# Performance work log

Hardware: AMD Instinct MI355X
Metric: run time of the kernel (lower is better)

The kernel has to match this reference:

```python
import jax, jax.numpy as jnp
import numpy as np

N = 50000      # nodes
E = 800000     # edges (avg degree 16)
G = 1024       # graphs in batch
C = 128        # hidden / interaction channels
FIN = 16       # num_node_features
FE = 3         # num_edge_features
L = 3          # num_interactions
CUTOFF = 10.0
LOG2 = float(np.log(2.0))
BN_EPS = 1e-5

def ssp(v):
    # ShiftedSoftplus: softplus(x) - log(2)
    return jax.nn.softplus(v) - LOG2

def setup_inputs() -> dict:
    key = jax.random.key(0)
    ks = jax.random.split(key, 24)
    s = 0.05
    inp = {}
    inp["x"] = jax.random.normal(ks[0], (N, FIN), jnp.float32)
    inp["edge_index"] = jax.random.randint(ks[1], (2, E), 0, N, dtype=jnp.int32)
    inp["edge_weight"] = jax.random.uniform(ks[2], (E,), jnp.float32) * CUTOFF
    inp["edge_attr"] = jax.random.normal(ks[3], (E, FE), jnp.float32)
    inp["batch"] = jnp.sort(jax.random.randint(ks[4], (N,), 0, G, dtype=jnp.int32))
    # node embedding (node_data='x'): Linear(FIN,C) -> Linear(C,C)
    inp["W_l1"] = jax.random.normal(ks[5], (FIN, C), jnp.float32) * s
    inp["b_l1"] = jnp.zeros((C,), jnp.float32)
    inp["W_l2"] = jax.random.normal(ks[6], (C, C), jnp.float32) * s
    inp["b_l2"] = jnp.zeros((C,), jnp.float32)
    # BatchNorm1d affine params
    inp["bn_g"] = jnp.ones((C,), jnp.float32)
    inp["bn_b"] = jnp.zeros((C,), jnp.float32)
    # L stacked interaction layers (SchNet-style CFConv)
    inp["Wi_in"] = jax.random.normal(ks[7], (L, C, C), jnp.float32) * s
    inp["bi_in"] = jnp.zeros((L, C), jnp.float32)
    inp["We1"] = jax.random.normal(ks[8], (L, FE, C), jnp.float32) * s
    inp["be1"] = jnp.zeros((L, C), jnp.float32)
    inp["We2"] = jax.random.normal(ks[9], (L, C, C), jnp.float32) * s
    inp["be2"] = jnp.zeros((L, C), jnp.float32)
    inp["Wi_out"] = jax.random.normal(ks[10], (L, C, C), jnp.float32) * s
    inp["bi_out"] = jnp.zeros((L, C), jnp.float32)
    # GeneralReadOutLayer (128,'sum',32,1): pool -> Linear(128,32)+SSP -> Linear(32,1)+SSP
    inp["W_r1"] = jax.random.normal(ks[11], (C, 32), jnp.float32) * s
    inp["b_r1"] = jnp.zeros((32,), jnp.float32)
    inp["W_r2"] = jax.random.normal(ks[12], (32, 1), jnp.float32) * s
    inp["b_r2"] = jnp.zeros((1,), jnp.float32)
    return inp

def _forward(x, edge_weight, edge_attr,
             W_l1, b_l1, W_l2, b_l2, bn_g, bn_b,
             Wi_in, bi_in, We1, be1, We2, be2, Wi_out, bi_out,
             W_r1, b_r1, W_r2, b_r2, edge_index, batch):
    src, dst = edge_index[0], edge_index[1]
    # node embedding: Linear -> Linear
    h = (x @ W_l1 + b_l1) @ W_l2 + b_l2                   # [N, C]
    # BatchNorm1d (training-mode batch stats over nodes)
    mu = jnp.mean(h, axis=0)
    var = jnp.var(h, axis=0)
    h = (h - mu) * jax.lax.rsqrt(var + BN_EPS) * bn_g + bn_b
    # cosine cutoff envelope on edge distances
    env = 0.5 * (jnp.cos(edge_weight * (jnp.pi / CUTOFF)) + 1.0)  # [E]
    # GeoResNet: residual stack of interactions
    for i in range(L):
        filt = ssp(edge_attr @ We1[i] + be1[i]) @ We2[i] + be2[i]   # [E, C]
        hin = h @ Wi_in[i] + bi_in[i]                               # [N, C]
        msg = hin[src] * filt * env[:, None]                        # [E, C] gather
        agg = jax.ops.segment_sum(msg, dst, num_segments=N)         # [N, C] scatter
        h = h + ssp(agg @ Wi_out[i] + bi_out[i])
    # GeneralReadOutLayer: segment 'sum' pool then MLP with SSP
    hg = jax.ops.segment_sum(h, batch, num_segments=G)              # [G, C]
    out = ssp(hg @ W_r1 + b_r1)
    out = ssp(out @ W_r2 + b_r2)                                    # [G, 1]
    return out.reshape(-1)                                          # [G]

def reference(x, edge_index, edge_weight, edge_attr, batch,
              W_l1, b_l1, W_l2, b_l2, bn_g, bn_b,
              Wi_in, bi_in, We1, be1, We2, be2, Wi_out, bi_out,
              W_r1, b_r1, W_r2, b_r2):
    return _forward(x, edge_weight, edge_attr,
                    W_l1, b_l1, W_l2, b_l2, bn_g, bn_b,
                    Wi_in, bi_in, We1, be1, We2, be2, Wi_out, bi_out,
                    W_r1, b_r1, W_r2, b_r2, edge_index, batch)
```

## Files before the change

### kernel.cpp

```cpp
#include <hip/hip_runtime.h>
#include <math.h>

#define N_NODES 50000
#define N_EDGES 800000
#define N_GRAPH 1024
#define CDIM 128
#define FINDIM 16
#define NL 3
#define WTP 132

using short8  = __attribute__((ext_vector_type(8))) short;
using floatx4 = __attribute__((ext_vector_type(4))) float;

__device__ __forceinline__ float sspf(float x) {
    return fmaxf(x, 0.0f) + __logf(1.0f + __expf(-fabsf(x))) - 0.6931471805599453f;
}

__device__ __forceinline__ unsigned short f2bf(float f) {
    unsigned int u = __float_as_uint(f);
    u = u + 0x7FFFu + ((u >> 16) & 1u);
    return (unsigned short)(u >> 16);
}

__device__ __forceinline__ float bf2f(unsigned short h) {
    return __uint_as_float((unsigned int)h << 16);
}

__device__ __forceinline__ short8 ldfrag(const unsigned short* WT, int c, int k0) {
    const uint2* p = (const uint2*)(WT + c * WTP + k0);
    short8 r;
    *(uint2*)&r       = p[0];
    *((uint2*)&r + 1) = p[1];
    return r;
}

__global__ void k_fuse(const float* __restrict__ Wl1, const float* __restrict__ bl1,
                       const float* __restrict__ Wl2, const float* __restrict__ bl2,
                       float* __restrict__ Wf, float* __restrict__ bfv) {
    for (int o = threadIdx.x; o < FINDIM * CDIM + CDIM; o += 256) {
        if (o < FINDIM * CDIM) {
            int f = o >> 7, c = o & 127;
            float s = 0.f;
            for (int k = 0; k < CDIM; ++k) s += Wl1[f * CDIM + k] * Wl2[k * CDIM + c];
            Wf[o] = s;
        } else {
            int c = o - FINDIM * CDIM;
            float s = bl2[c];
            for (int k = 0; k < CDIM; ++k) s += bl1[k] * Wl2[k * CDIM + c];
            bfv[c] = s;
        }
    }
}

__global__ void k_embed_bn(const float* __restrict__ x, const float* __restrict__ Wf,
                           const float* __restrict__ bfv, float* __restrict__ h,
                           float* __restrict__ bnsum) {
    __shared__ float wfs[FINDIM * CDIM];
    __shared__ float bfs[CDIM];
    __shared__ float sd[512];
    for (int o = threadIdx.x; o < FINDIM * CDIM; o += 256) wfs[o] = Wf[o];
    if (threadIdx.x < CDIM) bfs[threadIdx.x] = bfv[threadIdx.x];
    __syncthreads();
    int c = threadIdx.x & 127;
    int half = threadIdx.x >> 7;
    float s1 = 0.f, s2 = 0.f;
    for (int base = blockIdx.x * 2; base < N_NODES; base += gridDim.x * 2) {
        int n = base + half;
        if (n < N_NODES) {
            float s = bfs[c];
            const float* xp = x + (size_t)n * FINDIM;
#pragma unroll
            for (int f = 0; f < FINDIM; ++f) s += xp[f] * wfs[f * CDIM + c];
            h[(size_t)n * CDIM + c] = s;
            s1 += s; s2 += s * s;
        }
    }
    sd[threadIdx.x] = s1; sd[256 + threadIdx.x] = s2;
    __syncthreads();
    if (threadIdx.x < 128) {
        atomicAdd(&bnsum[threadIdx.x], sd[threadIdx.x] + sd[threadIdx.x + 128]);
        atomicAdd(&bnsum[128 + threadIdx.x], sd[256 + threadIdx.x] + sd[256 + threadIdx.x + 128]);
    }
}

__global__ void k_bnapply(float* __restrict__ h, unsigned short* __restrict__ hb,
                          const float* __restrict__ bnsum,
                          const float* __restrict__ g, const float* __restrict__ b) {
    const float invN = 1.0f / (float)N_NODES;
    for (size_t i = (size_t)blockIdx.x * 256 + threadIdx.x; i < (size_t)N_NODES * CDIM;
         i += (size_t)gridDim.x * 256) {
        int c = (int)(i & 127);
        float mu  = bnsum[c] * invN;
        float var = bnsum[128 + c] * invN - mu * mu;
        float sc  = g[c] * rsqrtf(var + 1e-5f);
        float v = (h[i] - mu) * sc + b[c];
        h[i] = v;
        hb[i] = f2bf(v);
    }
}

__global__ void k_hist(const int* __restrict__ edst, int* __restrict__ deg) {
    int e = blockIdx.x * 256 + threadIdx.x;
    if (e < N_EDGES) atomicAdd(&deg[edst[e]], 1);
}

#define SCAN_T 1024
#define CHUNK 49
__global__ void k_scan(const int* __restrict__ deg, int* __restrict__ row_ptr) {
    __shared__ int part[SCAN_T];
    int t = threadIdx.x;
    int begin = t * CHUNK;
    int end   = begin + CHUNK; if (end > N_NODES) end = N_NODES;
    int s = 0;
    for (int i = begin; i < end && i < N_NODES; ++i) s += deg[i];
    part[t] = s;
    __syncthreads();
    for (int off = 1; off < SCAN_T; off <<= 1) {
        int v = (t >= off) ? part[t - off] : 0;
        __syncthreads();
        part[t] += v;
        __syncthreads();
    }
    int run = (t == 0) ? 0 : part[t - 1];
    for (int i = begin; i < end && i < N_NODES; ++i) { row_ptr[i] = run; run += deg[i]; }
    if (t == SCAN_T - 1) row_ptr[N_NODES] = run;
}

__global__ void k_scatter(const int* __restrict__ edst, const int* __restrict__ row_ptr,
                          int* __restrict__ cnt, int* __restrict__ perm) {
    int e = blockIdx.x * 256 + threadIdx.x;
    if (e < N_EDGES) {
        int d = edst[e];
        int pos = row_ptr[d] + atomicAdd(&cnt[d], 1);
        perm[pos] = e;
    }
}

__global__ void k_pack(const int* __restrict__ perm, const int* __restrict__ esrc,
                       const int* __restrict__ edst, const float* __restrict__ ew,
                       const float* __restrict__ ea,
                       int2* __restrict__ rmeta, float4* __restrict__ rea) {
    int i = blockIdx.x * 256 + threadIdx.x;
    if (i < N_EDGES) {
        int e = perm[i];
        float w = ew[e];
        float env = 0.5f * (__cosf(w * 0.31415926535897932f) + 1.0f);
        rmeta[i] = make_int2(esrc[e], edst[e]);
        rea[i] = make_float4(ea[(size_t)e * 3], ea[(size_t)e * 3 + 1], ea[(size_t)e * 3 + 2], env);
    }
}

__global__ __launch_bounds__(256, 2) void k_ngemm_in(const unsigned short* __restrict__ hb,
                                                     const float* __restrict__ B,
                                                     const float* __restrict__ bias,
                                                     unsigned short* __restrict__ hinb) {
    __shared__ unsigned short WT[128 * WTP];
    __shared__ float bs[CDIM];
    for (int o = threadIdx.x; o < CDIM * CDIM; o += 256) {
        int k = o >> 7, c = o & 127;
        WT[c * WTP + k] = f2bf(B[o]);
    }
    if (threadIdx.x < CDIM) bs[threadIdx.x] = bias[threadIdx.x];
    __syncthreads();

    int lane = threadIdx.x & 63, wave = threadIdx.x >> 6;
    int m = lane & 15, q = lane >> 4;
    int rb = blockIdx.x * 64 + wave * 16;
    int row = rb + m;
    if (row > N_NODES - 1) row = N_NODES - 1;

    floatx4 acc[8];
#pragma unroll
    for (int nt = 0; nt < 8; ++nt) acc[nt] = (floatx4){0.f, 0.f, 0.f, 0.f};

#pragma unroll
    for (int kb = 0; kb < 4; ++kb) {
        int k0 = kb * 32 + q * 8;
        short8 af = *(const short8*)(hb + (size_t)row * CDIM + k0);
#pragma unroll
        for (int nt = 0; nt < 8; ++nt) {
            short8 bf = ldfrag(WT, nt * 16 + m, k0);
            acc[nt] = __builtin_amdgcn_mfma_f32_16x16x32_bf16(af, bf, acc[nt], 0, 0, 0);
        }
    }
#pragma unroll
    for (int nt = 0; nt < 8; ++nt) {
        int c = nt * 16 + m;
#pragma unroll
        for (int r = 0; r < 4; ++r) {
            int orow = rb + q * 4 + r;
            if (orow < N_NODES)
                hinb[(size_t)orow * CDIM + c] = f2bf(acc[nt][r] + bs[c]);
        }
    }
}

template <int ZERO, int POOL>
__global__ __launch_bounds__(256, 2) void k_ngemm_out(float* __restrict__ agg,
                                                      const float* __restrict__ B,
                                                      const float* __restrict__ bias,
                                                      float* __restrict__ h,
                                                      unsigned short* __restrict__ hb,
                                                      const int* __restrict__ batch,
                                                      float* __restrict__ hg) {
    __shared__ unsigned short WT[128 * WTP];
    __shared__ float bs[CDIM];
    for (int o = threadIdx.x; o < CDIM * CDIM; o += 256) {
        int k = o >> 7, c = o & 127;
        WT[c * WTP + k] = f2bf(B[o]);
    }
    if (threadIdx.x < CDIM) bs[threadIdx.x] = bias[threadIdx.x];
    __syncthreads();

    int lane = threadIdx.x & 63, wave = threadIdx.x >> 6;
    int m = lane & 15, q = lane >> 4;
    int rb = blockIdx.x * 64 + wave * 16;
    int row = rb + m;
    if (row > N_NODES - 1) row = N_NODES - 1;

    floatx4 acc[8];
#pragma unroll
    for (int nt = 0; nt < 8; ++nt) acc[nt] = (floatx4){0.f, 0.f, 0.f, 0.f};

#pragma unroll
    for (int kb = 0; kb < 4; ++kb) {
        int k0 = kb * 32 + q * 8;
        const float* ap = agg + (size_t)row * CDIM + k0;
        float4 lo = *(const float4*)ap;
        float4 hi = *(const float4*)(ap + 4);
        short8 af;
        af[0] = (short)f2bf(lo.x); af[1] = (short)f2bf(lo.y);
        af[2] = (short)f2bf(lo.z); af[3] = (short)f2bf(lo.w);
        af[4] = (short)f2bf(hi.x); af[5] = (short)f2bf(hi.y);
        af[6] = (short)f2bf(hi.z); af[7] = (short)f2bf(hi.w);
#pragma unroll
        for (int nt = 0; nt < 8; ++nt) {
            short8 bf = ldfrag(WT, nt * 16 + m, k0);
            acc[nt] = __builtin_amdgcn_mfma_f32_16x16x32_bf16(af, bf, acc[nt], 0, 0, 0);
        }
    }

    int batchr[4];
    if (POOL) {
#pragma unroll
        for (int r = 0; r < 4; ++r) {
            int orow = rb + q * 4 + r;
            batchr[r] = (orow < N_NODES) ? batch[orow] : 0;
        }
    }
#pragma unroll
    for (int nt = 0; nt < 8; ++nt) {
        int c = nt * 16 + m;
#pragma unroll
        for (int r = 0; r < 4; ++r) {
            int orow = rb + q * 4 + r;
            if (orow < N_NODES) {
                size_t idx = (size_t)orow * CDIM + c;
                float hn = h[idx] + sspf(acc[nt][r] + bs[c]);
                if (POOL) {
                    atomicAdd(&hg[(size_t)batchr[r] * CDIM + c], hn);
                } else {
                    h[idx] = hn;
                    hb[idx] = f2bf(hn);
                }
                if (ZERO) agg[idx] = 0.f;
            }
        }
    }
}

__global__ __launch_bounds__(256, 4) void k_edge(
    const float* __restrict__ We1, const float* __restrict__ be1,
    const float* __restrict__ We2, const float* __restrict__ be2,
    const int2* __restrict__ rmeta, const float4* __restrict__ rea,
    const unsigned short* __restrict__ hin, float* __restrict__ agg) {
    __shared__ unsigned short WT[128 * WTP];
    __shared__ float we1s[3 * CDIM];
    __shared__ float be1s[CDIM];
    __shared__ float be2s[CDIM];
    __shared__ int2   sds[64];
    __shared__ float4 eas4[64];

    for (int o = threadIdx.x; o < CDIM * CDIM; o += 256) {
        int k = o >> 7, c = o & 127;
        WT[c * WTP + k] = f2bf(We2[o]);
    }
    for (int o = threadIdx.x; o < 3 * CDIM; o += 256) we1s[o] = We1[o];
    if (threadIdx.x < CDIM) { be1s[threadIdx.x] = be1[threadIdx.x]; be2s[threadIdx.x] = be2[threadIdx.x]; }
    __syncthreads();

    int lane = threadIdx.x & 63, wave = threadIdx.x >> 6;
    int m = lane & 15, q = lane >> 4;

    const int ntiles = N_EDGES / 64;
    int tpb = (ntiles + gridDim.x - 1) / gridDim.x;
    int t0 = blockIdx.x * tpb;
    int t1 = t0 + tpb; if (t1 > ntiles) t1 = ntiles;

    for (int tile = t0; tile < t1; ++tile) {
        int s0 = tile * 64;
        __syncthreads();
        if (threadIdx.x < 64)       sds[threadIdx.x]        = rmeta[s0 + threadIdx.x];
        else if (threadIdx.x < 128) eas4[threadIdx.x - 64]  = rea[s0 + threadIdx.x - 64];
        __syncthreads();

        int el0 = wave * 16 + q * 4;
        int2 sd[4]; float ev[4];
#pragma unroll
        for (int r = 0; r < 4; ++r) { sd[r] = sds[el0 + r]; ev[r] = eas4[el0 + r].w; }

        unsigned short hpre[4][8];
#pragma unroll
        for (int r = 0; r < 4; ++r) {
            const unsigned short* hp = hin + (size_t)sd[r].x * CDIM + m;
#pragma unroll
            for (int nt = 0; nt < 8; ++nt) hpre[r][nt] = hp[nt * 16];
        }

        float4 eav = eas4[wave * 16 + m];
        float ea0 = eav.x, ea1 = eav.y, ea2 = eav.z;
        short8 af[4];
#pragma unroll
        for (int kb = 0; kb < 4; ++kb) {
#pragma unroll
            for (int jj = 0; jj < 4; ++jj) {
                int k = kb * 32 + q * 8 + jj * 2;
                float p0 = fmaf(we1s[k], ea0, fmaf(we1s[CDIM + k], ea1,
                             fmaf(we1s[2 * CDIM + k], ea2, be1s[k])));
                float p1 = fmaf(we1s[k + 1], ea0, fmaf(we1s[CDIM + k + 1], ea1,
                             fmaf(we1s[2 * CDIM + k + 1], ea2, be1s[k + 1])));
                unsigned int pk = (unsigned int)f2bf(sspf(p0)) |
                                  ((unsigned int)f2bf(sspf(p1)) << 16);
                ((unsigned int*)&af[kb])[jj] = pk;
            }
        }

        floatx4 acc[8];
#pragma unroll
        for (int nt = 0; nt < 8; ++nt) acc[nt] = (floatx4){0.f, 0.f, 0.f, 0.f};
#pragma unroll
        for (int kb = 0; kb < 4; ++kb)
#pragma unroll
            for (int nt = 0; nt < 8; ++nt) {
                short8 bf = ldfrag(WT, nt * 16 + m, kb * 32 + q * 8);
                acc[nt] = __builtin_amdgcn_mfma_f32_16x16x32_bf16(af[kb], bf, acc[nt], 0, 0, 0);
            }

        bool uni = (sd[0].y == sd[3].y);
        float vv[8];
#pragma unroll
        for (int nt = 0; nt < 8; ++nt) {
            float bias = be2s[nt * 16 + m];
            float s = 0.f;
#pragma unroll
            for (int r = 0; r < 4; ++r)
                s += (acc[nt][r] + bias) * ev[r] * bf2f(hpre[r][nt]);
            vv[nt] = s;
        }

        int owner = uni ? 1 : 0;
        int myd   = uni ? sd[0].y : -1 - lane;
#pragma unroll
        for (int s = 16; s <= 32; s <<= 1) {
            int od = __shfl_xor(myd, s, 64);
            int oo = __shfl_xor(owner, s, 64);
            bool match = owner && oo && (od == myd);
            bool lower = ((lane & s) == 0);
#pragma unroll
            for (int nt = 0; nt < 8; ++nt) {
                float ovv = __shfl_xor(vv[nt], s, 64);
                if (match && lower) vv[nt] += ovv;
            }
            if (match && !lower) { owner = 0; myd = -1 - lane; }
        }

        if (uni) {
            if (owner) {
                float* ap = agg + (size_t)myd * CDIM + m;
#pragma unroll
                for (int nt = 0; nt < 8; ++nt) atomicAdd(&ap[nt * 16], vv[nt]);
            }
        } else {
#pragma unroll
            for (int nt = 0; nt < 8; ++nt) {
                int c = nt * 16 + m;
                float bias = be2s[c];
                int cur = sd[0].y;
                float accv = (acc[nt][0] + bias) * ev[0] * bf2f(hpre[0][nt]);
#pragma unroll
                for (int r = 1; r < 4; ++r) {
                    float msg = (acc[nt][r] + bias) * ev[r] * bf2f(hpre[r][nt]);
                    if (sd[r].y != cur) {
                        atomicAdd(&agg[(size_t)cur * CDIM + c], accv);
                        cur = sd[r].y; accv = msg;
                    } else {
                        accv += msg;
                    }
                }
                atomicAdd(&agg[(size_t)cur * CDIM + c], accv);
            }
        }
    }
}

__global__ void k_readout(const float* __restrict__ hg, const float* __restrict__ Wr1,
                          const float* __restrict__ br1, const float* __restrict__ Wr2,
                          const float* __restrict__ br2, float* __restrict__ out) {
    __shared__ float hgs[CDIM];
    int g = blockIdx.x;
    for (int o = threadIdx.x; o < CDIM; o += 64) hgs[o] = hg[(size_t)g * CDIM + o];
    __syncthreads();
    int c = threadIdx.x;
    float val = 0.f;
    if (c < 32) {
        float s = br1[c];
        for (int k = 0; k < CDIM; ++k) s += hgs[k] * Wr1[k * 32 + c];
        val = sspf(s) * Wr2[c];
    }
#pragma unroll
    for (int off = 16; off >= 1; off >>= 1) val += __shfl_down(val, off, 32);
    if (c == 0) out[g] = sspf(val + br2[0]);
}

extern "C" void kernel_launch(void* const* d_in, const int* in_sizes, int n_in,
                              void* d_out, int out_size, void* d_ws, size_t ws_size,
                              hipStream_t stream) {
    const float* x     = (const float*)d_in[0];
    const int*   eidx  = (const int*)  d_in[1];
    const float* ew    = (const float*)d_in[2];
    const float* ea    = (const float*)d_in[3];
    const int*   batch = (const int*)  d_in[4];
    const float* Wl1   = (const float*)d_in[5];
    const float* bl1   = (const float*)d_in[6];
    const float* Wl2   = (const float*)d_in[7];
    const float* bl2   = (const float*)d_in[8];
    const float* bng   = (const float*)d_in[9];
    const float* bnb   = (const float*)d_in[10];
    const float* Wi_in = (const float*)d_in[11];
    const float* bi_in = (const float*)d_in[12];
    const float* We1   = (const float*)d_in[13];
    const float* be1   = (const float*)d_in[14];
    const float* We2   = (const float*)d_in[15];
    const float* be2   = (const float*)d_in[16];
    const float* Wi_o  = (const float*)d_in[17];
    const float* bi_o  = (const float*)d_in[18];
    const float* Wr1   = (const float*)d_in[19];
    const float* br1   = (const float*)d_in[20];
    const float* Wr2   = (const float*)d_in[21];
    const float* br2   = (const float*)d_in[22];
    float* out = (float*)d_out;

    float* ws  = (float*)d_ws;
    float*  h    = ws;
    float*  agg  = h + (size_t)N_NODES * CDIM;
    float4* rea  = (float4*)(agg + (size_t)N_NODES * CDIM);
    float*  hg   = (float*)(rea + N_EDGES);
    float*  Wf   = hg + (size_t)N_GRAPH * CDIM;
    float*  bfv  = Wf + FINDIM * CDIM;
    float*  bnsum = bfv + CDIM;
    unsigned short* hb   = (unsigned short*)(bnsum + 256);
    unsigned short* hinb = hb + (size_t)N_NODES * CDIM;
    int2*  rmeta  = (int2*)(hinb + (size_t)N_NODES * CDIM);
    int*   perm   = (int*)(rmeta + N_EDGES);
    int*   deg    = perm + N_EDGES;
    int*   row_ptr= deg + N_NODES;
    int*   cnt    = row_ptr + N_NODES + 1;

    const int* esrc = eidx;
    const int* edst = eidx + N_EDGES;

    hipMemsetAsync(deg, 0, (size_t)N_NODES * sizeof(int), stream);
    hipMemsetAsync(cnt, 0, (size_t)N_NODES * sizeof(int), stream);
    k_hist<<<(N_EDGES + 255) / 256, 256, 0, stream>>>(edst, deg);
    k_scan<<<1, SCAN_T, 0, stream>>>(deg, row_ptr);
    k_scatter<<<(N_EDGES + 255) / 256, 256, 0, stream>>>(edst, row_ptr, cnt, perm);
    k_pack<<<(N_EDGES + 255) / 256, 256, 0, stream>>>(perm, esrc, edst, ew, ea, rmeta, rea);

    hipMemsetAsync(bnsum, 0, 256 * sizeof(float), stream);
    k_fuse<<<1, 256, 0, stream>>>(Wl1, bl1, Wl2, bl2, Wf, bfv);
    k_embed_bn<<<512, 256, 0, stream>>>(x, Wf, bfv, h, bnsum);
    k_bnapply<<<1024, 256, 0, stream>>>(h, hb, bnsum, bng, bnb);

    hipMemsetAsync(agg, 0, (size_t)N_NODES * CDIM * sizeof(float), stream);
    hipMemsetAsync(hg, 0, (size_t)N_GRAPH * CDIM * sizeof(float), stream);
    const int ngrid = (N_NODES + 63) / 64;
    for (int l = 0; l < NL; ++l) {
        k_ngemm_in<<<ngrid, 256, 0, stream>>>(hb, Wi_in + (size_t)l * CDIM * CDIM,
                                              bi_in + l * CDIM, hinb);
        k_edge<<<1024, 256, 0, stream>>>(We1 + l * 3 * CDIM, be1 + l * CDIM,
                                         We2 + (size_t)l * CDIM * CDIM, be2 + l * CDIM,
                                         rmeta, rea, hinb, agg);
        if (l < NL - 1)
            k_ngemm_out<1, 0><<<ngrid, 256, 0, stream>>>(agg, Wi_o + (size_t)l * CDIM * CDIM,
                                                         bi_o + l * CDIM, h, hb, batch, hg);
        else
            k_ngemm_out<0, 1><<<ngrid, 256, 0, stream>>>(agg, Wi_o + (size_t)l * CDIM * CDIM,
                                                         bi_o + l * CDIM, h, hb, batch, hg);
    }

    k_readout<<<N_GRAPH, 64, 0, stream>>>(hg, Wr1, br1, Wr2, br2, out);
}
```

Measured before the change: 946.6 us.

## Drop per-tile LDS staging and barriers in edge kernel, fold biases, use packed bf16 convert

The edge kernel no longer stages edge metadata into shared memory behind two barriers per tile. Each lane now loads its src/dst and edge attributes directly from global memory. The first-layer weights and bias are interleaved into float4 in LDS, and the second-layer bias now initialises the MFMA accumulators instead of being added afterwards. Float-to-bf16 conversion uses the packed hardware intrinsic, and softplus is simplified to log(1+exp(x)), which can overflow for large inputs. The trade is redundant global loads per lane in exchange for removing the synchronisation.

```diff
diff --git a/kernel.cpp b/kernel.cpp
--- a/kernel.cpp
+++ b/kernel.cpp
@@ -1,4 +1,5 @@
 #include <hip/hip_runtime.h>
+#include <hip/hip_bf16.h>
 #include <math.h>
 
 #define N_NODES 50000
@@ -13,7 +14,7 @@
 using floatx4 = __attribute__((ext_vector_type(4))) float;
 
 __device__ __forceinline__ float sspf(float x) {
-    return fmaxf(x, 0.0f) + __logf(1.0f + __expf(-fabsf(x))) - 0.6931471805599453f;
+    return __logf(1.0f + __expf(x)) - 0.6931471805599453f;
 }
 
 __device__ __forceinline__ unsigned short f2bf(float f) {
@@ -24,6 +25,11 @@
 
 __device__ __forceinline__ float bf2f(unsigned short h) {
     return __uint_as_float((unsigned int)h << 16);
+}
+
+__device__ __forceinline__ unsigned int packbf(float a, float b) {
+    __hip_bfloat162 h = __float22bfloat162_rn(make_float2(a, b));
+    return *(unsigned int*)&h;
 }
 
 __device__ __forceinline__ short8 ldfrag(const unsigned short* WT, int c, int k0) {
@@ -229,10 +235,10 @@
         float4 lo = *(const float4*)ap;
         float4 hi = *(const float4*)(ap + 4);
         short8 af;
-        af[0] = (short)f2bf(lo.x); af[1] = (short)f2bf(lo.y);
-        af[2] = (short)f2bf(lo.z); af[3] = (short)f2bf(lo.w);
-        af[4] = (short)f2bf(hi.x); af[5] = (short)f2bf(hi.y);
-        af[6] = (short)f2bf(hi.z); af[7] = (short)f2bf(hi.w);
+        ((unsigned int*)&af)[0] = packbf(lo.x, lo.y);
+        ((unsigned int*)&af)[1] = packbf(lo.z, lo.w);
+        ((unsigned int*)&af)[2] = packbf(hi.x, hi.y);
+        ((unsigned int*)&af)[3] = packbf(hi.z, hi.w);
 #pragma unroll
         for (int nt = 0; nt < 8; ++nt) {
             short8 bf = ldfrag(WT, nt * 16 + m, k0);
@@ -275,39 +281,45 @@
     const int2* __restrict__ rmeta, const float4* __restrict__ rea,
     const unsigned short* __restrict__ hin, float* __restrict__ agg) {
     __shared__ unsigned short WT[128 * WTP];
-    __shared__ float we1s[3 * CDIM];
-    __shared__ float be1s[CDIM];
+    __shared__ float4 we1i[CDIM];
     __shared__ float be2s[CDIM];
-    __shared__ int2   sds[64];
-    __shared__ float4 eas4[64];
 
     for (int o = threadIdx.x; o < CDIM * CDIM; o += 256) {
         int k = o >> 7, c = o & 127;
         WT[c * WTP + k] = f2bf(We2[o]);
     }
-    for (int o = threadIdx.x; o < 3 * CDIM; o += 256) we1s[o] = We1[o];
-    if (threadIdx.x < CDIM) { be1s[threadIdx.x] = be1[threadIdx.x]; be2s[threadIdx.x] = be2[threadIdx.x]; }
+    if (threadIdx.x < CDIM) {
+        int k = threadIdx.x;
+        we1i[k] = make_float4(We1[k], We1[CDIM + k], We1[2 * CDIM + k], be1[k]);
+        be2s[k] = be2[k];
+    }
     __syncthreads();
 
     int lane = threadIdx.x & 63, wave = threadIdx.x >> 6;
     int m = lane & 15, q = lane >> 4;
+
+    float biasr[8];
+#pragma unroll
+    for (int nt = 0; nt < 8; ++nt) biasr[nt] = be2s[nt * 16 + m];
 
     const int ntiles = N_EDGES / 64;
     int tpb = (ntiles + gridDim.x - 1) / gridDim.x;
     int t0 = blockIdx.x * tpb;
     int t1 = t0 + tpb; if (t1 > ntiles) t1 = ntiles;
 
+    const float* reaf = (const float*)rea;
+
     for (int tile = t0; tile < t1; ++tile) {
         int s0 = tile * 64;
-        __syncthreads();
-        if (threadIdx.x < 64)       sds[threadIdx.x]        = rmeta[s0 + threadIdx.x];
-        else if (threadIdx.x < 128) eas4[threadIdx.x - 64]  = rea[s0 + threadIdx.x - 64];
-        __syncthreads();
-
         int el0 = wave * 16 + q * 4;
+
         int2 sd[4]; float ev[4];
 #pragma unroll
-        for (int r = 0; r < 4; ++r) { sd[r] = sds[el0 + r]; ev[r] = eas4[el0 + r].w; }
+        for (int r = 0; r < 4; ++r) {
+            sd[r] = rmeta[s0 + el0 + r];
+            ev[r] = reaf[(size_t)(s0 + el0 + r) * 4 + 3];
+        }
+        float4 eav = rea[s0 + wave * 16 + m];
 
         unsigned short hpre[4][8];
 #pragma unroll
@@ -317,7 +329,6 @@
             for (int nt = 0; nt < 8; ++nt) hpre[r][nt] = hp[nt * 16];
         }
 
-        float4 eav = eas4[wave * 16 + m];
         float ea0 = eav.x, ea1 = eav.y, ea2 = eav.z;
         short8 af[4];
 #pragma unroll
@@ -325,19 +336,18 @@
 #pragma unroll
             for (int jj = 0; jj < 4; ++jj) {
                 int k = kb * 32 + q * 8 + jj * 2;
-                float p0 = fmaf(we1s[k], ea0, fmaf(we1s[CDIM + k], ea1,
-                             fmaf(we1s[2 * CDIM + k], ea2, be1s[k])));
-                float p1 = fmaf(we1s[k + 1], ea0, fmaf(we1s[CDIM + k + 1], ea1,
-                             fmaf(we1s[2 * CDIM + k + 1], ea2, be1s[k + 1])));
-                unsigned int pk = (unsigned int)f2bf(sspf(p0)) |
-                                  ((unsigned int)f2bf(sspf(p1)) << 16);
-                ((unsigned int*)&af[kb])[jj] = pk;
+                float4 w0 = we1i[k];
+                float4 w1 = we1i[k + 1];
+                float p0 = fmaf(w0.x, ea0, fmaf(w0.y, ea1, fmaf(w0.z, ea2, w0.w)));
+                float p1 = fmaf(w1.x, ea0, fmaf(w1.y, ea1, fmaf(w1.z, ea2, w1.w)));
+                ((unsigned int*)&af[kb])[jj] = packbf(sspf(p0), sspf(p1));
             }
         }
 
         floatx4 acc[8];
 #pragma unroll
-        for (int nt = 0; nt < 8; ++nt) acc[nt] = (floatx4){0.f, 0.f, 0.f, 0.f};
+        for (int nt = 0; nt < 8; ++nt)
+            acc[nt] = (floatx4){biasr[nt], biasr[nt], biasr[nt], biasr[nt]};
 #pragma unroll
         for (int kb = 0; kb < 4; ++kb)
 #pragma unroll
@@ -350,11 +360,10 @@
         float vv[8];
 #pragma unroll
         for (int nt = 0; nt < 8; ++nt) {
-            float bias = be2s[nt * 16 + m];
             float s = 0.f;
 #pragma unroll
             for (int r = 0; r < 4; ++r)
-                s += (acc[nt][r] + bias) * ev[r] * bf2f(hpre[r][nt]);
+                s += acc[nt][r] * ev[r] * bf2f(hpre[r][nt]);
             vv[nt] = s;
         }
 
@@ -384,12 +393,11 @@
 #pragma unroll
             for (int nt = 0; nt < 8; ++nt) {
                 int c = nt * 16 + m;
-                float bias = be2s[c];
                 int cur = sd[0].y;
-                float accv = (acc[nt][0] + bias) * ev[0] * bf2f(hpre[0][nt]);
+                float accv = acc[nt][0] * ev[0] * bf2f(hpre[0][nt]);
 #pragma unroll
                 for (int r = 1; r < 4; ++r) {
-                    float msg = (acc[nt][r] + bias) * ev[r] * bf2f(hpre[r][nt]);
+                    float msg = acc[nt][r] * ev[r] * bf2f(hpre[r][nt]);
                     if (sd[r].y != cur) {
                         atomicAdd(&agg[(size_t)cur * CDIM + c], accv);
                         cur = sd[r].y; accv = msg;
```

After: 2.733 ms. 189% more time.
